# Kernel tuning notes

Measured on AMD Instinct MI355X. Metric: run time of the kernel, lower is better.

The kernel has to match this reference:

```python
import jax, jax.numpy as jnp
import numpy as np

DIM = 768
NUM_HEADS = 12
HEAD_DIM = DIM // NUM_HEADS
SCALE = HEAD_DIM ** -0.5
NEG = -9e15


def setup_inputs() -> dict:
    key = jax.random.key(0)
    ks = jax.random.split(key, 8)
    B, N, M, C = 4, 1024, 2048, DIM
    q = jax.random.normal(ks[0], (B, N, C), dtype=jnp.float32)
    kv = jax.random.normal(ks[1], (B, M, C), dtype=jnp.float32)
    mask = jax.random.randint(ks[2], (B, 1, N, M), 0, 2, dtype=jnp.int32)
    s = 1.0 / np.sqrt(C)
    Wq = jax.random.normal(ks[3], (C, C), dtype=jnp.float32) * s      # nn.Linear(dim, dim), no bias
    Wkv = jax.random.normal(ks[4], (2 * C, C), dtype=jnp.float32) * s  # nn.Linear(dim, 2*dim), no bias
    Wproj = jax.random.normal(ks[5], (C, C), dtype=jnp.float32) * s
    bproj = jax.random.normal(ks[6], (C,), dtype=jnp.float32) * s
    return {"q": q, "kv": kv, "Wq": Wq, "Wkv": Wkv, "Wproj": Wproj, "bproj": bproj, "mask": mask}


def reference(q, kv, Wq, Wkv, Wproj, bproj, mask):
    B, M, C = kv.shape
    _, N, _ = q.shape
    H, d = NUM_HEADS, HEAD_DIM
    # kv projection -> [B, M, 2, H, d] -> k, v: [B, H, M, d]
    kvp = (kv @ Wkv.T).reshape(B, M, 2, H, d)
    k = kvp[:, :, 0].transpose(0, 2, 1, 3)
    v = kvp[:, :, 1].transpose(0, 2, 1, 3)
    # q projection -> [B, H, N, d], pre-scaled
    qp = (q @ Wq.T).reshape(B, N, H, d).transpose(0, 2, 1, 3) * SCALE
    attn = jnp.einsum('bhnd,bhmd->bhnm', qp, k)  # [B, H, N, M]
    attn = jnp.where(mask == 0, NEG, attn)
    attn = jax.nn.softmax(attn, axis=-1)
    # attn_drop / proj_drop have rate 0.0 (eval): identity
    x = jnp.einsum('bhnm,bhmd->bhnd', attn, v)
    x = x.transpose(0, 2, 1, 3).reshape(B, N, C)
    x = x @ Wproj.T + bproj
    return x
```

## Files before the change

### kernel.cpp

```cpp
#include <hip/hip_runtime.h>
#include <hip/hip_bf16.h>


typedef short    s16x8  __attribute__((ext_vector_type(8)));
typedef short    s16x4  __attribute__((ext_vector_type(4)));
typedef float    f32x4  __attribute__((ext_vector_type(4)));
typedef _Float16 f16x8  __attribute__((ext_vector_type(8)));
typedef _Float16 f16x4  __attribute__((ext_vector_type(4)));
typedef _Float16 f16x2  __attribute__((ext_vector_type(2)));

#define NUM_H 12
#define DIM   768
#define NQ    1024
#define MK    2048
#define QK_SCALE_LOG2E 0.18033688f

__device__ __forceinline__ short f2h(float v) {
    _Float16 h = (_Float16)v;
    return __builtin_bit_cast(short, h);
}
__device__ __forceinline__ f32x4 mfma16x32(f16x8 a, f16x8 b, f32x4 c) {
    return __builtin_amdgcn_mfma_f32_16x16x32_f16(a, b, c, 0, 0, 0);
}
__device__ __forceinline__ f16x2 pk2h(float a, float b) {
    return __builtin_bit_cast(f16x2, __builtin_amdgcn_cvt_pkrtz(a, b));
}

__global__ __launch_bounds__(256) void prep_kernel(
    const float* __restrict__ q, const float* __restrict__ kv,
    const float* __restrict__ Wq, const float* __restrict__ Wkv,
    const float* __restrict__ Wp, const int* __restrict__ mask,
    short* __restrict__ q_h, short* __restrict__ kv_h,
    short* __restrict__ Wq_h, short* __restrict__ Wkv_h,
    short* __restrict__ Wp_h, unsigned char* __restrict__ mbytes)
{
    int bid = blockIdx.x;
    if (bid < 5760) {
        const float* s; short* d; long base;
        if (bid < 1536)      { s = q;   d = q_h;   base = (long)bid * 2048; }
        else if (bid < 4608) { s = kv;  d = kv_h;  base = (long)(bid - 1536) * 2048; }
        else if (bid < 4896) { s = Wq;  d = Wq_h;  base = (long)(bid - 4608) * 2048; }
        else if (bid < 5472) { s = Wkv; d = Wkv_h; base = (long)(bid - 4896) * 2048; }
        else                 { s = Wp;  d = Wp_h;  base = (long)(bid - 5472) * 2048; }
        long i = base + threadIdx.x * 8;
        float4 a = *(const float4*)(s + i);
        float4 b = *(const float4*)(s + i + 4);
        s16x8 r;
        r[0] = f2h(a.x); r[1] = f2h(a.y); r[2] = f2h(a.z); r[3] = f2h(a.w);
        r[4] = f2h(b.x); r[5] = f2h(b.y); r[6] = f2h(b.z); r[7] = f2h(b.w);
        *(s16x8*)(d + i) = r;
    } else {
        long base = (long)(bid - 5760) * 2048 + threadIdx.x * 8;
        int4 m0 = *(const int4*)(mask + base);
        int4 m1 = *(const int4*)(mask + base + 4);
        unsigned v = (unsigned)(m0.x != 0)        | ((unsigned)(m0.y != 0) << 1)
                   | ((unsigned)(m0.z != 0) << 2) | ((unsigned)(m0.w != 0) << 3)
                   | ((unsigned)(m1.x != 0) << 4) | ((unsigned)(m1.y != 0) << 5)
                   | ((unsigned)(m1.z != 0) << 6) | ((unsigned)(m1.w != 0) << 7);
        mbytes[base >> 3] = (unsigned char)v;
    }
}

__device__ __forceinline__ void gemm_core(
    short* smem,
    const short* __restrict__ A, const short* __restrict__ Bt,
    int Ncols, int mode, const float* __restrict__ bias,
    short* __restrict__ outb, short* __restrict__ outb2,
    float* __restrict__ outf, int bid)
{
    int ntiles = Ncols >> 7;
    int m0 = (bid / ntiles) << 7;
    int n0 = (bid % ntiles) << 7;
    int t = threadIdx.x;
    int w = t >> 6, lane = t & 63, quad = lane >> 4, l16 = lane & 15;
    int wm = (w & 1) << 6, wn = (w >> 1) << 6;

    f32x4 zero4 = {0.f, 0.f, 0.f, 0.f};
    f32x4 acc[4][4];
    for (int i = 0; i < 4; i++)
        for (int j = 0; j < 4; j++) acc[i][j] = zero4;

    int srow = (w << 3) + (lane >> 3);
    int scol = (((lane & 7) ^ (lane >> 3)) << 3);
    const short* Asrc = A + (long)(m0 + srow) * DIM + scol;
    const short* Bsrc = Bt + (long)(n0 + srow) * DIM + scol;
    int dstoff = (w << 9) + (lane << 3);

    auto stage = [&](short* bufA, short* bufB, int kt) {
        #pragma unroll
        for (int i = 0; i < 4; i++) {
            __builtin_amdgcn_global_load_lds(
                (const unsigned int*)(Asrc + (long)i * 32 * DIM + kt),
                (unsigned int*)(bufA + dstoff + i * 2048), 16, 0, 0);
            __builtin_amdgcn_global_load_lds(
                (const unsigned int*)(Bsrc + (long)i * 32 * DIM + kt),
                (unsigned int*)(bufB + dstoff + i * 2048), 16, 0, 0);
        }
    };

    int swl = l16 & 7;

    stage(smem, smem + 8192, 0);
    __syncthreads();

    for (int kt = 0; kt < DIM; kt += 64) {
        short* Ac = smem + ((kt & 64) ? 16384 : 0);
        short* Bc = Ac + 8192;
        if (kt + 64 < DIM) {
            short* An = smem + ((kt & 64) ? 0 : 16384);
            stage(An, An + 8192, kt + 64);
        }
        #pragma unroll
        for (int kh = 0; kh < 2; kh++) {
            f16x8 af[4], bfr[4];
            #pragma unroll
            for (int i = 0; i < 4; i++)
                af[i] = __builtin_bit_cast(f16x8, *(const s16x8*)(
                    Ac + ((wm + i * 16 + l16) << 6)
                       + ((((kh << 2) | quad) ^ swl) << 3)));
            #pragma unroll
            for (int j = 0; j < 4; j++)
                bfr[j] = __builtin_bit_cast(f16x8, *(const s16x8*)(
                    Bc + ((wn + j * 16 + l16) << 6)
                       + ((((kh << 2) | quad) ^ swl) << 3)));
            #pragma unroll
            for (int i = 0; i < 4; i++)
                #pragma unroll
                for (int j = 0; j < 4; j++)
                    acc[i][j] = mfma16x32(af[i], bfr[j], acc[i][j]);
        }
        __syncthreads();
    }

    if (mode == 2) {
        #pragma unroll
        for (int i = 0; i < 4; i++)
            #pragma unroll
            for (int j = 0; j < 4; j++)
                #pragma unroll
                for (int r = 0; r < 4; r++) {
                    int row = m0 + wm + i * 16 + quad * 4 + r;
                    int col = n0 + wn + j * 16 + l16;
                    outf[(long)row * DIM + col] = acc[i][j][r] + bias[col];
                }
        return;
    }

    short (*Cs)[136] = (short(*)[136])smem;
    bool vreg = (mode == 1) && (n0 >= DIM);

    if (!vreg) {
        float sc = (mode == 0) ? QK_SCALE_LOG2E : 1.0f;
        #pragma unroll
        for (int i = 0; i < 4; i++)
            #pragma unroll
            for (int j = 0; j < 4; j++)
                #pragma unroll
                for (int r = 0; r < 4; r++)
                    Cs[wm + i * 16 + quad * 4 + r][wn + j * 16 + l16] =
                        f2h(acc[i][j][r] * sc);
    } else {
        #pragma unroll
        for (int i = 0; i < 4; i++)
            #pragma unroll
            for (int j = 0; j < 4; j++) {
                int c = wn + j * 16 + l16;
                int r0 = wm + i * 16 + quad * 4;
                s16x4 pk;
                pk[0] = f2h(acc[i][j][0]); pk[1] = f2h(acc[i][j][1]);
                pk[2] = f2h(acc[i][j][2]); pk[3] = f2h(acc[i][j][3]);
                *(s16x4*)&Cs[c][r0] = pk;
            }
    }
    __syncthreads();

    if (!vreg) {
        int hb2 = n0 >> 6;
        long rowsN = (mode == 0) ? NQ : MK;
        int b = (int)(m0 / rowsN);
        int rb = (int)(m0 % rowsN);
        short* ob0 = outb + ((long)(b * NUM_H + hb2) * rowsN + rb) * 64;
        short* ob1 = outb + ((long)(b * NUM_H + hb2 + 1) * rowsN + rb) * 64;
        #pragma unroll
        for (int k2 = 0; k2 < 8; k2++) {
            int ch = k2 * 256 + t;
            int half = ch >> 10, off = ch & 1023;
            s16x8 vd = *(const s16x8*)&Cs[off >> 3][(half << 6) + ((off & 7) << 3)];
            *(s16x8*)((half ? ob1 : ob0) + off * 8) = vd;
        }
    } else {
        int hb2 = (n0 - DIM) >> 6;
        int b = m0 >> 11, rb = m0 & 2047;
        #pragma unroll
        for (int k2 = 0; k2 < 8; k2++) {
            int ch = k2 * 256 + t;
            int c = ch >> 4, woff = (ch & 15) << 3;
            s16x8 vd = *(const s16x8*)&Cs[c][woff];
            int half = c >> 6, dd = c & 63;
            *(s16x8*)(outb2 + (((long)(b * NUM_H + hb2 + half) * 64 + dd) * MK + rb) + woff) = vd;
        }
    }
}

__global__ __launch_bounds__(256) void gemm12_kernel(
    const short* __restrict__ qh, const short* __restrict__ Wqh,
    const short* __restrict__ kvh, const short* __restrict__ Wkvh,
    short* __restrict__ qp, short* __restrict__ kk, short* __restrict__ vt)
{
    __shared__ short smem[32768];
    if (blockIdx.x < 192)
        gemm_core(smem, qh, Wqh, 768, 0, nullptr, qp, nullptr, nullptr, blockIdx.x);
    else
        gemm_core(smem, kvh, Wkvh, 1536, 1, nullptr, kk, vt, nullptr, blockIdx.x - 192);
}

__global__ __launch_bounds__(256) void gemm3_kernel(
    const short* __restrict__ xb, const short* __restrict__ Wph,
    const float* __restrict__ bias, float* __restrict__ out)
{
    __shared__ short smem[32768];
    gemm_core(smem, xb, Wph, 768, 2, bias, nullptr, nullptr, out, blockIdx.x);
}

__global__ __launch_bounds__(256) void attn_kernel(
    const short* __restrict__ qp, const short* __restrict__ kk,
    const short* __restrict__ vt, const unsigned* __restrict__ mb,
    short* __restrict__ xb)
{
    __shared__ short qs[64][72];
    __shared__ short ks[64][64];
    __shared__ short vs[64][64];

    int bid = blockIdx.x;
    int bh = bid % 48;
    int nt = bid / 48;
    int h = bh % NUM_H, b = bh / NUM_H;
    int n0 = nt << 6;
    int t = threadIdx.x, w = t >> 6, lane = t & 63, quad = lane >> 4, l16 = lane & 15;

    const short* qbase = qp + ((long)bh * NQ + n0) * 64;
    const short* kbase = kk + (long)bh * MK * 64;
    const short* vbase = vt + (long)bh * 64 * MK;
    const unsigned* mrow = mb + ((long)b * NQ + n0 + (w << 4) + l16) * 64;

    {
        int qr = t >> 2, c0q = (t & 3) << 4;
        *(s16x8*)&qs[qr][c0q]     = *(const s16x8*)(qbase + qr * 64 + c0q);
        *(s16x8*)&qs[qr][c0q + 8] = *(const s16x8*)(qbase + qr * 64 + c0q + 8);
    }
    __syncthreads();
    f16x8 bq[2];
    #pragma unroll
    for (int kh = 0; kh < 2; kh++)
        bq[kh] = __builtin_bit_cast(f16x8,
            *(const s16x8*)&qs[(w << 4) + l16][kh * 32 + quad * 8]);

    int sr = t >> 2, c0 = (t & 3) << 4;
    int pr = (sr & 32) + ((sr & 4) << 2) + ((sr & 24) >> 1) + (sr & 3);
    int swk = (pr & 7) << 3;
    int swv = (sr & 7) << 3;
    int swl = (l16 & 7) << 3;
    const short* kp = kbase + (long)sr * 64 + c0;
    const short* vp = vbase + (long)sr * MK + c0;

    s16x8 k0 = *(const s16x8*)(kp);
    s16x8 k1 = *(const s16x8*)(kp + 8);
    s16x8 v0 = *(const s16x8*)(vp);
    s16x8 v1 = *(const s16x8*)(vp + 8);
    uint2 mwv = *(const uint2*)(mrow);

    f32x4 zero4 = {0.f, 0.f, 0.f, 0.f};
    f32x4 o[4], ol = zero4;
    for (int j = 0; j < 4; j++) o[j] = zero4;
    const f16x8 ones = {(_Float16)1.f, (_Float16)1.f, (_Float16)1.f, (_Float16)1.f,
                        (_Float16)1.f, (_Float16)1.f, (_Float16)1.f, (_Float16)1.f};

    for (int mt = 0; mt < MK; mt += 64) {
        __syncthreads();
        *(s16x8*)&ks[pr][c0 ^ swk]       = k0;
        *(s16x8*)&ks[pr][(c0 + 8) ^ swk] = k1;
        *(s16x8*)&vs[sr][c0 ^ swv]       = v0;
        *(s16x8*)&vs[sr][(c0 + 8) ^ swv] = v1;
        unsigned cm0 = mwv.x, cm1 = mwv.y;
        __syncthreads();
        if (mt + 64 < MK) {
            k0 = *(const s16x8*)(kp + (long)(mt + 64) * 64);
            k1 = *(const s16x8*)(kp + (long)(mt + 64) * 64 + 8);
            v0 = *(const s16x8*)(vp + mt + 64);
            v1 = *(const s16x8*)(vp + mt + 64 + 8);
            mwv = *(const uint2*)(mrow + ((mt + 64) >> 5));
        }

        f32x4 s[4];
        #pragma unroll
        for (int jj = 0; jj < 4; jj++) s[jj] = zero4;
        __builtin_amdgcn_s_setprio(1);
        #pragma unroll
        for (int kh = 0; kh < 2; kh++)
            #pragma unroll
            for (int jj = 0; jj < 4; jj++) {
                f16x8 ak = __builtin_bit_cast(f16x8,
                    *(const s16x8*)&ks[jj * 16 + l16][(kh * 32 + quad * 8) ^ swl]);
                s[jj] = mfma16x32(ak, bq[kh], s[jj]);
            }
        __builtin_amdgcn_s_setprio(0);

        f16x8 pa[2];
        #pragma unroll
        for (int j2 = 0; j2 < 2; j2++) {
            unsigned wsel = j2 ? cm1 : cm0;
            f16x2 pk[4];
            #pragma unroll
            for (int sub = 0; sub < 2; sub++) {
                unsigned bits = wsel >> ((quad << 3) + (sub << 2));
                const f32x4& sv = s[j2 * 2 + sub];
                float p0 = (bits & 1u)        ? __builtin_amdgcn_exp2f(sv[0]) : 0.f;
                float p1 = ((bits >> 1) & 1u) ? __builtin_amdgcn_exp2f(sv[1]) : 0.f;
                float p2 = ((bits >> 2) & 1u) ? __builtin_amdgcn_exp2f(sv[2]) : 0.f;
                float p3 = ((bits >> 3) & 1u) ? __builtin_amdgcn_exp2f(sv[3]) : 0.f;
                pk[sub * 2]     = pk2h(p0, p1);
                pk[sub * 2 + 1] = pk2h(p2, p3);
            }
            f16x4 lo = __builtin_shufflevector(pk[0], pk[1], 0, 1, 2, 3);
            f16x4 hi = __builtin_shufflevector(pk[2], pk[3], 0, 1, 2, 3);
            pa[j2] = __builtin_shufflevector(lo, hi, 0, 1, 2, 3, 4, 5, 6, 7);
        }

        __builtin_amdgcn_s_setprio(1);
        #pragma unroll
        for (int j2 = 0; j2 < 2; j2++) {
            ol = mfma16x32(pa[j2], ones, ol);
            #pragma unroll
            for (int jd = 0; jd < 4; jd++) {
                f16x8 bv = __builtin_bit_cast(f16x8,
                    *(const s16x8*)&vs[jd * 16 + l16][(j2 * 32 + quad * 8) ^ swl]);
                o[jd] = mfma16x32(pa[j2], bv, o[jd]);
            }
        }
        __builtin_amdgcn_s_setprio(0);
    }

    float linv[4];
    #pragma unroll
    for (int rr = 0; rr < 4; rr++) linv[rr] = 1.0f / ol[rr];
    short (*ps)[72] = (short(*)[72])&qs[w << 4];
    #pragma unroll
    for (int jd = 0; jd < 4; jd++)
        #pragma unroll
        for (int rr = 0; rr < 4; rr++)
            ps[quad * 4 + rr][jd * 16 + l16] = f2h(o[jd][rr] * linv[rr]);

    #pragma unroll
    for (int k2 = 0; k2 < 2; k2++) {
        int row = (lane >> 3) + k2 * 8;
        int cc = (lane & 7) << 3;
        s16x8 vd = *(const s16x8*)&ps[row][cc];
        *(s16x8*)(xb + ((long)b * NQ + n0 + (w << 4) + row) * DIM + h * 64 + cc) = vd;
    }
}

extern "C" void kernel_launch(void* const* d_in, const int* in_sizes, int n_in,
                              void* d_out, int out_size, void* d_ws, size_t ws_size,
                              hipStream_t stream)
{
    const float* q     = (const float*)d_in[0];
    const float* kv    = (const float*)d_in[1];
    const float* Wq    = (const float*)d_in[2];
    const float* Wkv   = (const float*)d_in[3];
    const float* Wproj = (const float*)d_in[4];
    const float* bproj = (const float*)d_in[5];
    const int*   mask  = (const int*)d_in[6];
    float* out = (float*)d_out;

    char* ws = (char*)d_ws;
    short* q_h   = (short*)ws; ws += (size_t)4096 * 768 * 2;
    short* kv_h  = (short*)ws; ws += (size_t)8192 * 768 * 2;
    short* Wq_h  = (short*)ws; ws += (size_t)768 * 768 * 2;
    short* Wkv_h = (short*)ws; ws += (size_t)1536 * 768 * 2;
    short* Wp_h  = (short*)ws; ws += (size_t)768 * 768 * 2;
    short* qp    = (short*)ws; ws += (size_t)4096 * 768 * 2;
    short* kk    = (short*)ws; ws += (size_t)8192 * 768 * 2;
    short* vt    = (short*)ws; ws += (size_t)8192 * 768 * 2;
    short* xb    = (short*)ws; ws += (size_t)4096 * 768 * 2;
    unsigned char* mbytes = (unsigned char*)ws;

    prep_kernel<<<9856, 256, 0, stream>>>(q, kv, Wq, Wkv, Wproj, mask,
                                          q_h, kv_h, Wq_h, Wkv_h, Wp_h, mbytes);
    gemm12_kernel<<<960, 256, 0, stream>>>(q_h, Wq_h, kv_h, Wkv_h, qp, kk, vt);
    attn_kernel<<<768, 256, 0, stream>>>(qp, kk, vt, (const unsigned*)mbytes, xb);
    gemm3_kernel<<<192, 256, 0, stream>>>(xb, Wp_h, bproj, out);
}
```

Measured before the change: 209.6 us.

## Give each attention wave two 16-row query tiles, halving block size

The attention kernel now runs 128 threads (2 waves) per block, and each wave handles 32 query rows as two 16-row sub-tiles instead of 16 rows. Every K and V fragment read from shared memory feeds two MFMAs, which halves LDS reads per unit of compute. Each thread also loads twice as much K/V staging data from global memory per tile. The cost is roughly double the accumulator and staging registers per thread and fewer waves per block to hide latency, which may lower occupancy.

Result: slower. 216.6 us (+3.3%).

```diff
diff --git a/kernel.cpp b/kernel.cpp
--- a/kernel.cpp
+++ b/kernel.cpp
@@ -222,7 +222,7 @@
     gemm_core(smem, xb, Wph, 768, 2, bias, nullptr, nullptr, out, blockIdx.x);
 }
 
-__global__ __launch_bounds__(256) void attn_kernel(
+__global__ __launch_bounds__(128) void attn_kernel(
     const short* __restrict__ qp, const short* __restrict__ kk,
     const short* __restrict__ vt, const unsigned* __restrict__ mb,
     short* __restrict__ xb)
@@ -241,21 +241,26 @@
     const short* qbase = qp + ((long)bh * NQ + n0) * 64;
     const short* kbase = kk + (long)bh * MK * 64;
     const short* vbase = vt + (long)bh * 64 * MK;
-    const unsigned* mrow = mb + ((long)b * NQ + n0 + (w << 4) + l16) * 64;
+    const unsigned* mrow0 = mb + ((long)b * NQ + n0 + (w << 5) + l16) * 64;
+    const unsigned* mrow1 = mrow0 + 16 * 64;
 
     {
-        int qr = t >> 2, c0q = (t & 3) << 4;
-        *(s16x8*)&qs[qr][c0q]     = *(const s16x8*)(qbase + qr * 64 + c0q);
-        *(s16x8*)&qs[qr][c0q + 8] = *(const s16x8*)(qbase + qr * 64 + c0q + 8);
+        int qr = t >> 1, c0q = (t & 1) << 5;
+        #pragma unroll
+        for (int i = 0; i < 4; i++)
+            *(s16x8*)&qs[qr][c0q + i * 8] =
+                *(const s16x8*)(qbase + qr * 64 + c0q + i * 8);
     }
     __syncthreads();
-    f16x8 bq[2];
+    f16x8 bq[2][2];
     #pragma unroll
-    for (int kh = 0; kh < 2; kh++)
-        bq[kh] = __builtin_bit_cast(f16x8,
-            *(const s16x8*)&qs[(w << 4) + l16][kh * 32 + quad * 8]);
-
-    int sr = t >> 2, c0 = (t & 3) << 4;
+    for (int qa = 0; qa < 2; qa++)
+        #pragma unroll
+        for (int kh = 0; kh < 2; kh++)
+            bq[qa][kh] = __builtin_bit_cast(f16x8,
+                *(const s16x8*)&qs[(w << 5) + (qa << 4) + l16][kh * 32 + quad * 8]);
+
+    int sr = t >> 1, c0 = (t & 1) << 5;
     int pr = (sr & 32) + ((sr & 4) << 2) + ((sr & 24) >> 1) + (sr & 3);
     int swk = (pr & 7) << 3;
     int swv = (sr & 7) << 3;
@@ -263,37 +268,51 @@
     const short* kp = kbase + (long)sr * 64 + c0;
     const short* vp = vbase + (long)sr * MK + c0;
 
-    s16x8 k0 = *(const s16x8*)(kp);
-    s16x8 k1 = *(const s16x8*)(kp + 8);
-    s16x8 v0 = *(const s16x8*)(vp);
-    s16x8 v1 = *(const s16x8*)(vp + 8);
-    uint2 mwv = *(const uint2*)(mrow);
+    s16x8 kr[4], vr[4];
+    #pragma unroll
+    for (int c = 0; c < 4; c++) {
+        kr[c] = *(const s16x8*)(kp + c * 8);
+        vr[c] = *(const s16x8*)(vp + c * 8);
+    }
+    uint2 mwa = *(const uint2*)(mrow0);
+    uint2 mwb = *(const uint2*)(mrow1);
 
     f32x4 zero4 = {0.f, 0.f, 0.f, 0.f};
-    f32x4 o[4], ol = zero4;
-    for (int j = 0; j < 4; j++) o[j] = zero4;
+    f32x4 o[2][4], ol[2];
+    #pragma unroll
+    for (int qa = 0; qa < 2; qa++) {
+        ol[qa] = zero4;
+        for (int j = 0; j < 4; j++) o[qa][j] = zero4;
+    }
     const f16x8 ones = {(_Float16)1.f, (_Float16)1.f, (_Float16)1.f, (_Float16)1.f,
                         (_Float16)1.f, (_Float16)1.f, (_Float16)1.f, (_Float16)1.f};
 
     for (int mt = 0; mt < MK; mt += 64) {
         __syncthreads();
-        *(s16x8*)&ks[pr][c0 ^ swk]       = k0;
-        *(s16x8*)&ks[pr][(c0 + 8) ^ swk] = k1;
-        *(s16x8*)&vs[sr][c0 ^ swv]       = v0;
-        *(s16x8*)&vs[sr][(c0 + 8) ^ swv] = v1;
-        unsigned cm0 = mwv.x, cm1 = mwv.y;
+        #pragma unroll
+        for (int c = 0; c < 4; c++) {
+            *(s16x8*)&ks[pr][(c0 + c * 8) ^ swk] = kr[c];
+            *(s16x8*)&vs[sr][(c0 + c * 8) ^ swv] = vr[c];
+        }
+        uint2 cma = mwa, cmb = mwb;
         __syncthreads();
         if (mt + 64 < MK) {
-            k0 = *(const s16x8*)(kp + (long)(mt + 64) * 64);
-            k1 = *(const s16x8*)(kp + (long)(mt + 64) * 64 + 8);
-            v0 = *(const s16x8*)(vp + mt + 64);
-            v1 = *(const s16x8*)(vp + mt + 64 + 8);
-            mwv = *(const uint2*)(mrow + ((mt + 64) >> 5));
-        }
-
-        f32x4 s[4];
-        #pragma unroll
-        for (int jj = 0; jj < 4; jj++) s[jj] = zero4;
+            const short* kpn = kp + (long)(mt + 64) * 64;
+            const short* vpn = vp + mt + 64;
+            #pragma unroll
+            for (int c = 0; c < 4; c++) {
+                kr[c] = *(const s16x8*)(kpn + c * 8);
+                vr[c] = *(const s16x8*)(vpn + c * 8);
+            }
+            mwa = *(const uint2*)(mrow0 + ((mt + 64) >> 5));
+            mwb = *(const uint2*)(mrow1 + ((mt + 64) >> 5));
+        }
+
+        f32x4 s[2][4];
+        #pragma unroll
+        for (int qa = 0; qa < 2; qa++)
+            #pragma unroll
+            for (int jj = 0; jj < 4; jj++) s[qa][jj] = zero4;
         __builtin_amdgcn_s_setprio(1);
         #pragma unroll
         for (int kh = 0; kh < 2; kh++)
@@ -301,61 +320,73 @@
             for (int jj = 0; jj < 4; jj++) {
                 f16x8 ak = __builtin_bit_cast(f16x8,
                     *(const s16x8*)&ks[jj * 16 + l16][(kh * 32 + quad * 8) ^ swl]);
-                s[jj] = mfma16x32(ak, bq[kh], s[jj]);
+                s[0][jj] = mfma16x32(ak, bq[0][kh], s[0][jj]);
+                s[1][jj] = mfma16x32(ak, bq[1][kh], s[1][jj]);
             }
         __builtin_amdgcn_s_setprio(0);
 
-        f16x8 pa[2];
+        f16x8 pa[2][2];
+        #pragma unroll
+        for (int qa = 0; qa < 2; qa++) {
+            uint2 cm = qa ? cmb : cma;
+            #pragma unroll
+            for (int j2 = 0; j2 < 2; j2++) {
+                unsigned wsel = j2 ? cm.y : cm.x;
+                f16x2 pk[4];
+                #pragma unroll
+                for (int sub = 0; sub < 2; sub++) {
+                    unsigned bits = wsel >> ((quad << 3) + (sub << 2));
+                    const f32x4& sv = s[qa][j2 * 2 + sub];
+                    float p0 = (bits & 1u)        ? __builtin_amdgcn_exp2f(sv[0]) : 0.f;
+                    float p1 = ((bits >> 1) & 1u) ? __builtin_amdgcn_exp2f(sv[1]) : 0.f;
+                    float p2 = ((bits >> 2) & 1u) ? __builtin_amdgcn_exp2f(sv[2]) : 0.f;
+                    float p3 = ((bits >> 3) & 1u) ? __builtin_amdgcn_exp2f(sv[3]) : 0.f;
+                    pk[sub * 2]     = pk2h(p0, p1);
+                    pk[sub * 2 + 1] = pk2h(p2, p3);
+                }
+                f16x4 lo = __builtin_shufflevector(pk[0], pk[1], 0, 1, 2, 3);
+                f16x4 hi = __builtin_shufflevector(pk[2], pk[3], 0, 1, 2, 3);
+                pa[qa][j2] = __builtin_shufflevector(lo, hi, 0, 1, 2, 3, 4, 5, 6, 7);
+            }
+        }
+
+        __builtin_amdgcn_s_setprio(1);
         #pragma unroll
         for (int j2 = 0; j2 < 2; j2++) {
-            unsigned wsel = j2 ? cm1 : cm0;
-            f16x2 pk[4];
-            #pragma unroll
-            for (int sub = 0; sub < 2; sub++) {
-                unsigned bits = wsel >> ((quad << 3) + (sub << 2));
-                const f32x4& sv = s[j2 * 2 + sub];
-                float p0 = (bits & 1u)        ? __builtin_amdgcn_exp2f(sv[0]) : 0.f;
-                float p1 = ((bits >> 1) & 1u) ? __builtin_amdgcn_exp2f(sv[1]) : 0.f;
-                float p2 = ((bits >> 2) & 1u) ? __builtin_amdgcn_exp2f(sv[2]) : 0.f;
-                float p3 = ((bits >> 3) & 1u) ? __builtin_amdgcn_exp2f(sv[3]) : 0.f;
-                pk[sub * 2]     = pk2h(p0, p1);
-                pk[sub * 2 + 1] = pk2h(p2, p3);
-            }
-            f16x4 lo = __builtin_shufflevector(pk[0], pk[1], 0, 1, 2, 3);
-            f16x4 hi = __builtin_shufflevector(pk[2], pk[3], 0, 1, 2, 3);
-            pa[j2] = __builtin_shufflevector(lo, hi, 0, 1, 2, 3, 4, 5, 6, 7);
-        }
-
-        __builtin_amdgcn_s_setprio(1);
-        #pragma unroll
-        for (int j2 = 0; j2 < 2; j2++) {
-            ol = mfma16x32(pa[j2], ones, ol);
+            ol[0] = mfma16x32(pa[0][j2], ones, ol[0]);
+            ol[1] = mfma16x32(pa[1][j2], ones, ol[1]);
             #pragma unroll
             for (int jd = 0; jd < 4; jd++) {
                 f16x8 bv = __builtin_bit_cast(f16x8,
                     *(const s16x8*)&vs[jd * 16 + l16][(j2 * 32 + quad * 8) ^ swl]);
-                o[jd] = mfma16x32(pa[j2], bv, o[jd]);
+                o[0][jd] = mfma16x32(pa[0][j2], bv, o[0][jd]);
+                o[1][jd] = mfma16x32(pa[1][j2], bv, o[1][jd]);
             }
         }
         __builtin_amdgcn_s_setprio(0);
     }
 
-    float linv[4];
+    __syncthreads();
+    short (*ps)[72] = (short(*)[72])&qs[w << 5];
     #pragma unroll
-    for (int rr = 0; rr < 4; rr++) linv[rr] = 1.0f / ol[rr];
-    short (*ps)[72] = (short(*)[72])&qs[w << 4];
+    for (int qa = 0; qa < 2; qa++) {
+        float linv[4];
+        #pragma unroll
+        for (int rr = 0; rr < 4; rr++) linv[rr] = 1.0f / ol[qa][rr];
+        #pragma unroll
+        for (int jd = 0; jd < 4; jd++)
+            #pragma unroll
+            for (int rr = 0; rr < 4; rr++)
+                ps[(qa << 4) + quad * 4 + rr][jd * 16 + l16] =
+                    f2h(o[qa][jd][rr] * linv[rr]);
+    }
+
     #pragma unroll
-    for (int jd = 0; jd < 4; jd++)
-        #pragma unroll
-        for (int rr = 0; rr < 4; rr++)
-            ps[quad * 4 + rr][jd * 16 + l16] = f2h(o[jd][rr] * linv[rr]);
-
-    #pragma unroll
-    for (int k2 = 0; k2 < 2; k2++) {
+    for (int k2 = 0; k2 < 4; k2++) {
         int row = (lane >> 3) + k2 * 8;
         int cc = (lane & 7) << 3;
         s16x8 vd = *(const s16x8*)&ps[row][cc];
-        *(s16x8*)(xb + ((long)b * NQ + n0 + (w << 4) + row) * DIM + h * 64 + cc) = vd;
+        *(s16x8*)(xb + ((long)b * NQ + n0 + (w << 5) + row) * DIM + h * 64 + cc) = vd;
     }
 }
 
@@ -387,6 +418,6 @@
     prep_kernel<<<9856, 256, 0, stream>>>(q, kv, Wq, Wkv, Wproj, mask,
                                           q_h, kv_h, Wq_h, Wkv_h, Wp_h, mbytes);
     gemm12_kernel<<<960, 256, 0, stream>>>(q_h, Wq_h, kv_h, Wkv_h, qp, kk, vt);
-    attn_kernel<<<768, 256, 0, stream>>>(qp, kk, vt, (const unsigned*)mbytes, xb);
+    attn_kernel<<<768, 128, 0, stream>>>(qp, kk, vt, (const unsigned*)mbytes, xb);
     gemm3_kernel<<<192, 256, 0, stream>>>(xb, Wp_h, bproj, out);
 }
```
